# Performance work log

Hardware: AMD Instinct MI355X
Metric: run time of the kernel (lower is better)

Reference implementation:

```python
import jax, jax.numpy as jnp
import numpy as np

B, D, N = 2, 512, 2048
H, MQ, MV = 8, 64, 64
SCALE = 1.0 / np.sqrt(D).astype(np.float32)  # 1/sqrt(num_dim_q), full dim


def setup_inputs() -> dict:
    key = jax.random.key(0)
    ks = jax.random.split(key, 9)
    s = 0.02
    return {
        "Q": jax.random.normal(ks[0], (B, D, N), jnp.float32),
        "Wq": jax.random.normal(ks[1], (MQ * H, D), jnp.float32) * s,
        "bq": jnp.zeros((MQ * H,), jnp.float32),
        "Wk": jax.random.normal(ks[2], (MQ * H, D), jnp.float32) * s,
        "bk": jnp.zeros((MQ * H,), jnp.float32),
        "Wv": jax.random.normal(ks[3], (MV * H, D), jnp.float32) * s,
        "bv": jnp.zeros((MV * H,), jnp.float32),
        "Wo": jax.random.normal(ks[4], (D, MV * H), jnp.float32) * s,
        "bo": jnp.zeros((D,), jnp.float32),
    }


def _conv1x1(x, W, b):
    # Conv1d with kernel_size=1 == per-position linear: [B,Cin,N] -> [B,Cout,N]
    return jnp.einsum("bcn,oc->bon", x, W) + b[None, :, None]


def reference(Q, Wq, bq, Wk, bk, Wv, bv, Wo, bo):
    q = _conv1x1(Q, Wq, bq)  # [B, MQ*H, N]
    k = _conv1x1(Q, Wk, bk)
    v = _conv1x1(Q, Wv, bv)  # [B, MV*H, N]
    b = Q.shape[0]
    n = Q.shape[2]
    # channel index factors as (dim, head): channel = d*H + h (matches torch .view)
    q = q.reshape(b, MQ, H, n)
    k = k.reshape(b, MQ, H, n)
    v = v.reshape(b, MV, H, n)
    scores = jnp.einsum("bdhq,bdhk->bhqk", q, k) * SCALE  # [B,H,Nq,Nk]
    attn = jax.nn.softmax(scores, axis=-1)
    o = jnp.einsum("bhqk,bdhk->bdhq", attn, v)  # [B, MV, H, Nq]
    o = o.reshape(b, MV * H, n)
    return _conv1x1(o, Wo, bo)  # [B, D, N]
```

## Files before the change

### kernel.cpp

```cpp
#include <hip/hip_runtime.h>

#define DEV __device__ __forceinline__

typedef __bf16 bf16;
typedef __bf16 bf16x8 __attribute__((ext_vector_type(8)));
typedef __bf16 bf16x4 __attribute__((ext_vector_type(4)));
typedef float f32x4 __attribute__((ext_vector_type(4)));

#define B_ 2
#define D_ 512
#define N_ 2048
#define H_ 8
#define MD_ 64
#define SCALE_F (0.04419417382415922f * 1.4426950408889634f)

DEV void gload_lds16(const void* g, void* l) {
  __builtin_amdgcn_global_load_lds(
      (const __attribute__((address_space(1))) void*)g,
      (__attribute__((address_space(3))) void*)l, 16, 0, 0);
}

DEV f32x4 mfma16(bf16x8 a, bf16x8 b, f32x4 c) {
  return __builtin_amdgcn_mfma_f32_16x16x32_bf16(a, b, c, 0, 0, 0);
}

__global__ __launch_bounds__(256) void prep_w(
    const float* __restrict__ Wq, const float* __restrict__ bq,
    const float* __restrict__ Wk, const float* __restrict__ bk,
    const float* __restrict__ Wv, const float* __restrict__ bv,
    const float* __restrict__ Wo,
    bf16* __restrict__ Wf, float* __restrict__ biasf, bf16* __restrict__ Wor) {
  int row = blockIdx.x;
  int t = threadIdx.x;
  if (row < 1536) {
    const float* src;
    float scale = 1.0f;
    if (row < 512)       { src = Wq + (size_t)row * 512; scale = SCALE_F; }
    else if (row < 1024) { src = Wk + (size_t)(row - 512) * 512; }
    else                 { src = Wv + (size_t)(row - 1024) * 512; }
    for (int c = t; c < 512; c += 256)
      Wf[(size_t)row * 512 + c] = (bf16)(src[c] * scale);
    if (t == 0) {
      float bb;
      if (row < 512)       bb = bq[row] * SCALE_F;
      else if (row < 1024) bb = bk[row - 512];
      else                 bb = bv[row - 1024];
      biasf[row] = bb;
    }
  } else {
    int r = row - 1536;
    for (int c2 = t; c2 < 512; c2 += 256) {
      int hh = c2 >> 6, dd = c2 & 63;
      Wor[(size_t)r * 512 + c2] = (bf16)Wo[(size_t)r * 512 + dd * 8 + hh];
    }
  }
}

__global__ __launch_bounds__(256) void prep_qt(const float* __restrict__ Q,
                                               bf16* __restrict__ Qt) {
  __shared__ float tile[64][65];
  int b = blockIdx.z;
  int d0 = blockIdx.y * 64;
  int n0 = blockIdx.x * 64;
  int t = threadIdx.x;
  int r = t >> 2, cw = t & 3;

  const float* src = Q + ((size_t)(b * 512 + d0 + r)) * 2048 + n0 + cw * 16;
#pragma unroll
  for (int e4 = 0; e4 < 4; ++e4) {
    float4 v = *(const float4*)(src + e4 * 4);
    tile[r][cw * 16 + e4 * 4 + 0] = v.x;
    tile[r][cw * 16 + e4 * 4 + 1] = v.y;
    tile[r][cw * 16 + e4 * 4 + 2] = v.z;
    tile[r][cw * 16 + e4 * 4 + 3] = v.w;
  }
  __syncthreads();
  bf16x8 o0{}, o1{};
#pragma unroll
  for (int e = 0; e < 8; ++e) {
    o0[e] = (bf16)tile[cw * 16 + e][r];
    o1[e] = (bf16)tile[cw * 16 + 8 + e][r];
  }
  bf16* dst = Qt + ((size_t)(b * 2048 + n0 + r)) * 512 + d0 + cw * 16;
  *(bf16x8*)dst = o0;
  *((bf16x8*)dst + 1) = o1;
}

__global__ __launch_bounds__(256) void qkv_gemm(
    const bf16* __restrict__ Wf, const bf16* __restrict__ Qt,
    const float* __restrict__ biasf,
    bf16* __restrict__ qp, bf16* __restrict__ kp, bf16* __restrict__ vn) {
  __shared__ bf16 Al[128 * 32];
  __shared__ bf16 Bl[64 * 32];
  int b = blockIdx.z;
  int c0 = blockIdx.x * 128;
  int p0 = blockIdx.y * 64;
  int tid = threadIdx.x, w = tid >> 6, lane = tid & 63;
  int wm = w >> 1, wn = w & 1;
  int g = lane >> 4, l15 = lane & 15;

  const bf16* Abase = Wf + (size_t)c0 * 512;
  const bf16* Bbase = Qt + ((size_t)b * 2048 + p0) * 512;

  f32x4 acc[4][2] = {};

  for (int ks = 0; ks < 16; ++ks) {
    int k0 = ks * 32;
    __syncthreads();
#pragma unroll
    for (int i = 0; i < 2; ++i) {
      int rowl = w * 32 + i * 16 + (lane >> 2);
      gload_lds16(Abase + (size_t)rowl * 512 + k0 + (lane & 3) * 8,
                  Al + (w * 32 + i * 16) * 32);
    }
    {
      int browl = w * 16 + (lane >> 2);
      gload_lds16(Bbase + (size_t)browl * 512 + k0 + (lane & 3) * 8,
                  Bl + w * 16 * 32);
    }
    __syncthreads();
    bf16x8 a[4], bb[2];
#pragma unroll
    for (int mi = 0; mi < 4; ++mi)
      a[mi] = *(const bf16x8*)(Al + (wm * 64 + mi * 16 + l15) * 32 + g * 8);
#pragma unroll
    for (int ni = 0; ni < 2; ++ni)
      bb[ni] = *(const bf16x8*)(Bl + (wn * 32 + ni * 16 + l15) * 32 + g * 8);
#pragma unroll
    for (int mi = 0; mi < 4; ++mi)
#pragma unroll
      for (int ni = 0; ni < 2; ++ni)
        acc[mi][ni] = mfma16(a[mi], bb[ni], acc[mi][ni]);
  }

#pragma unroll
  for (int mi = 0; mi < 4; ++mi) {
#pragma unroll
    for (int ni = 0; ni < 2; ++ni) {
#pragma unroll
      for (int r = 0; r < 4; ++r) {
        int row = c0 + wm * 64 + mi * 16 + g * 4 + r;
        int p = p0 + wn * 32 + ni * 16 + l15;
        float val = acc[mi][ni][r] + biasf[row];
        bf16 hv = (bf16)val;
        if (row < 512) {
          int c = row;
          qp[(((size_t)b * 8 + (c & 7)) * 2048 + p) * 64 + (c >> 3)] = hv;
        } else if (row < 1024) {
          int c = row - 512;
          kp[(((size_t)b * 8 + (c & 7)) * 2048 + p) * 64 + (c >> 3)] = hv;
        } else {
          int c = row - 1024;
          vn[((size_t)b * 512 + c) * 2048 + p] = hv;
        }
      }
    }
  }
}

__global__ __launch_bounds__(512, 4) void attn_k(
    const bf16* __restrict__ qp, const bf16* __restrict__ kp,
    const bf16* __restrict__ vn, bf16* __restrict__ Op,
    float* __restrict__ mbuf, float* __restrict__ lbuf, int TS) {
  __shared__ bf16 Ks[2][64 * 64];
  __shared__ bf16 Vs[2][64 * 64];
  __shared__ bf16 Ps[256 * 64];
  int q0 = blockIdx.x * 256;
  int bh = blockIdx.y;
  int z = blockIdx.z;
  int b = bh >> 3, h = bh & 7;
  int tid = threadIdx.x, w = tid >> 6, lane = tid & 63;
  int g = lane >> 4, l15 = lane & 15;

  bf16x8 qreg[2][2];
#pragma unroll
  for (int rg = 0; rg < 2; ++rg)
#pragma unroll
    for (int ks2 = 0; ks2 < 2; ++ks2)
      qreg[rg][ks2] = *(const bf16x8*)(
          qp + ((size_t)bh * 2048 + q0 + w * 32 + rg * 16 + l15) * 64 +
          ks2 * 32 + g * 8);

  int krow = tid >> 3;
  int kch = (tid & 7) ^ (krow & 7);

  const bf16* Kall = kp + (size_t)bh * 2048 * 64 + (size_t)z * TS * 4096;
  const bf16* Vall = vn + ((size_t)(b * 512 + h)) * 2048 + (size_t)z * TS * 64;

  gload_lds16(Kall + (size_t)krow * 64 + kch * 8, Ks[0] + w * 512);
  gload_lds16(Vall + (size_t)krow * 16384 + kch * 8, Vs[0] + w * 512);

  f32x4 oacc[2][4] = {};
  float mrow[2] = {-1e30f, -1e30f}, rs[2] = {0.0f, 0.0f};

  __syncthreads();

  for (int t = 0; t < TS; ++t) {
    int cur = t & 1, nxt = cur ^ 1;
    int tn = (t < TS - 1) ? t + 1 : t;

    gload_lds16(Kall + (size_t)tn * 4096 + (size_t)krow * 64 + kch * 8,
                Ks[nxt] + w * 512);
    gload_lds16(Vall + (size_t)tn * 64 + (size_t)krow * 16384 + kch * 8,
                Vs[nxt] + w * 512);

    f32x4 st[2][4] = {};
    __builtin_amdgcn_s_setprio(1);
#pragma unroll
    for (int ks2 = 0; ks2 < 2; ++ks2) {
#pragma unroll
      for (int jt = 0; jt < 4; ++jt) {
        int jrow = jt * 16 + l15;
        bf16x8 kb = *(const bf16x8*)(Ks[cur] + jrow * 64 +
                                     (((ks2 * 4 + g) ^ (jrow & 7)) << 3));
        st[0][jt] = mfma16(kb, qreg[0][ks2], st[0][jt]);
        st[1][jt] = mfma16(kb, qreg[1][ks2], st[1][jt]);
      }
    }
    __builtin_amdgcn_s_setprio(0);

    float rm[2];
#pragma unroll
    for (int rg = 0; rg < 2; ++rg) {
      float m0 = st[rg][0][0];
#pragma unroll
      for (int jt = 0; jt < 4; ++jt)
#pragma unroll
        for (int i = 0; i < 4; ++i) m0 = fmaxf(m0, st[rg][jt][i]);
      m0 = fmaxf(m0, __shfl_xor(m0, 16));
      m0 = fmaxf(m0, __shfl_xor(m0, 32));
      rm[rg] = m0;
    }

    if (__any(fmaxf(rm[0] - mrow[0], rm[1] - mrow[1]) > 8.0f)) {
#pragma unroll
      for (int rg = 0; rg < 2; ++rg) {
        float nm = fmaxf(mrow[rg], rm[rg]);
        float esc = __builtin_amdgcn_exp2f(mrow[rg] - nm);
        mrow[rg] = nm;
        rs[rg] *= esc;
#pragma unroll
        for (int r = 0; r < 4; ++r) {
          float er = __shfl(esc, g * 4 + r, 64);
#pragma unroll
          for (int dt = 0; dt < 4; ++dt) oacc[rg][dt][r] *= er;
        }
      }
    }

#pragma unroll
    for (int rg = 0; rg < 2; ++rg) {
      int prow = w * 32 + rg * 16 + l15;
#pragma unroll
      for (int jt = 0; jt < 4; ++jt) {
        bf16x4 pk;
#pragma unroll
        for (int i = 0; i < 4; ++i) {
          float pv = __builtin_amdgcn_exp2f(st[rg][jt][i] - mrow[rg]);
          rs[rg] += pv;
          pk[i] = (bf16)pv;
        }
        *(bf16x4*)(Ps + prow * 64 + ((jt * 16 + g * 4) ^ ((prow & 7) << 3))) = pk;
      }
    }

    __builtin_amdgcn_s_setprio(1);
#pragma unroll
    for (int ks2 = 0; ks2 < 2; ++ks2) {
      int r0w = w * 32 + l15;
      int r1w = w * 32 + 16 + l15;
      bf16x8 pa0 = *(const bf16x8*)(Ps + r0w * 64 +
                                    (((ks2 * 4 + g) ^ (r0w & 7)) << 3));
      bf16x8 pa1 = *(const bf16x8*)(Ps + r1w * 64 +
                                    (((ks2 * 4 + g) ^ (r1w & 7)) << 3));
#pragma unroll
      for (int dt = 0; dt < 4; ++dt) {
        int drow = dt * 16 + l15;
        bf16x8 vb = *(const bf16x8*)(Vs[cur] + drow * 64 +
                                     (((ks2 * 4 + g) ^ (drow & 7)) << 3));
        oacc[0][dt] = mfma16(pa0, vb, oacc[0][dt]);
        oacc[1][dt] = mfma16(pa1, vb, oacc[1][dt]);
      }
    }
    __builtin_amdgcn_s_setprio(0);

    __syncthreads();
  }

#pragma unroll
  for (int rg = 0; rg < 2; ++rg) {
    rs[rg] += __shfl_xor(rs[rg], 16);
    rs[rg] += __shfl_xor(rs[rg], 32);
  }

  size_t zb = (size_t)(z * 16 + bh) * 2048 + q0;
#pragma unroll
  for (int rg = 0; rg < 2; ++rg) {
#pragma unroll
    for (int dt = 0; dt < 4; ++dt) {
#pragma unroll
      for (int r = 0; r < 4; ++r) {
        int i = w * 32 + rg * 16 + g * 4 + r;
        Op[(zb + i) * 64 + dt * 16 + l15] = (bf16)oacc[rg][dt][r];
      }
    }
  }
  if (lane < 16) {
#pragma unroll
    for (int rg = 0; rg < 2; ++rg) {
      int i = w * 32 + rg * 16 + l15;
      mbuf[zb + i] = mrow[rg];
      lbuf[zb + i] = rs[rg];
    }
  }
}

__global__ __launch_bounds__(256) void combine(
    const bf16* __restrict__ Op, const float* __restrict__ mbuf,
    const float* __restrict__ lbuf, bf16* __restrict__ oh, int NS) {
  int idx = blockIdx.x * 256 + threadIdx.x;
  int row = idx >> 2;
  int dc = (idx & 3) * 16;

  float M = -1e30f;
  for (int z = 0; z < NS; ++z) M = fmaxf(M, mbuf[(size_t)z * 32768 + row]);

  float L = 0.0f;
  float acc[16];
#pragma unroll
  for (int e = 0; e < 16; ++e) acc[e] = 0.0f;

  for (int z = 0; z < NS; ++z) {
    float wz = __builtin_amdgcn_exp2f(mbuf[(size_t)z * 32768 + row] - M);
    L += wz * lbuf[(size_t)z * 32768 + row];
    const bf16x8* p = (const bf16x8*)(Op + ((size_t)z * 32768 + row) * 64 + dc);
#pragma unroll
    for (int v = 0; v < 2; ++v) {
      bf16x8 x = p[v];
#pragma unroll
      for (int e = 0; e < 8; ++e) acc[v * 8 + e] += wz * (float)x[e];
    }
  }
  float invL = 1.0f / L;
  bf16x8* po = (bf16x8*)(oh + (size_t)row * 64 + dc);
#pragma unroll
  for (int v = 0; v < 2; ++v) {
    bf16x8 o;
#pragma unroll
    for (int e = 0; e < 8; ++e) o[e] = (bf16)(acc[v * 8 + e] * invL);
    po[v] = o;
  }
}

__global__ __launch_bounds__(256) void out_gemm(
    const bf16* __restrict__ Wor, const bf16* __restrict__ oh,
    const float* __restrict__ bo, float* __restrict__ out) {
  __shared__ bf16 Al[128 * 32];
  __shared__ bf16 Bl[64 * 32];
  int b = blockIdx.z;
  int r0 = blockIdx.x * 128;
  int p0 = blockIdx.y * 64;
  int tid = threadIdx.x, w = tid >> 6, lane = tid & 63;
  int wm = w >> 1, wn = w & 1;
  int g = lane >> 4, l15 = lane & 15;

  const bf16* Abase = Wor + (size_t)r0 * 512;

  f32x4 acc[4][2] = {};

  for (int ks = 0; ks < 16; ++ks) {
    int k0 = ks * 32;
    int hh = k0 >> 6, d0 = k0 & 63;
    const bf16* Bbase = oh + (((size_t)b * 8 + hh) * 2048 + p0) * 64 + d0;
    __syncthreads();
#pragma unroll
    for (int i = 0; i < 2; ++i) {
      int rowl = w * 32 + i * 16 + (lane >> 2);
      gload_lds16(Abase + (size_t)rowl * 512 + k0 + (lane & 3) * 8,
                  Al + (w * 32 + i * 16) * 32);
    }
    {
      int browl = w * 16 + (lane >> 2);
      gload_lds16(Bbase + (size_t)browl * 64 + (lane & 3) * 8,
                  Bl + w * 16 * 32);
    }
    __syncthreads();
    bf16x8 a[4], bb[2];
#pragma unroll
    for (int mi = 0; mi < 4; ++mi)
      a[mi] = *(const bf16x8*)(Al + (wm * 64 + mi * 16 + l15) * 32 + g * 8);
#pragma unroll
    for (int ni = 0; ni < 2; ++ni)
      bb[ni] = *(const bf16x8*)(Bl + (wn * 32 + ni * 16 + l15) * 32 + g * 8);
#pragma unroll
    for (int mi = 0; mi < 4; ++mi)
#pragma unroll
      for (int ni = 0; ni < 2; ++ni)
        acc[mi][ni] = mfma16(a[mi], bb[ni], acc[mi][ni]);
  }

#pragma unroll
  for (int mi = 0; mi < 4; ++mi) {
#pragma unroll
    for (int ni = 0; ni < 2; ++ni) {
#pragma unroll
      for (int r = 0; r < 4; ++r) {
        int row = r0 + wm * 64 + mi * 16 + g * 4 + r;
        int p = p0 + wn * 32 + ni * 16 + l15;
        out[((size_t)b * 512 + row) * 2048 + p] = acc[mi][ni][r] + bo[row];
      }
    }
  }
}

extern "C" void kernel_launch(void* const* d_in, const int* in_sizes, int n_in,
                              void* d_out, int out_size, void* d_ws, size_t ws_size,
                              hipStream_t stream) {
  (void)in_sizes; (void)n_in; (void)out_size;
  const float* Q  = (const float*)d_in[0];
  const float* Wq = (const float*)d_in[1];
  const float* bq = (const float*)d_in[2];
  const float* Wk = (const float*)d_in[3];
  const float* bk = (const float*)d_in[4];
  const float* Wv = (const float*)d_in[5];
  const float* bv = (const float*)d_in[6];
  const float* Wo = (const float*)d_in[7];
  const float* bo = (const float*)d_in[8];
  float* out = (float*)d_out;

  char* ws = (char*)d_ws;
  bf16*  Wf    = (bf16*)(ws + 0);
  bf16*  Wor   = (bf16*)(ws + 1572864);
  float* biasf = (float*)(ws + 2097152);
  bf16*  Qt    = (bf16*)(ws + 2103296);
  bf16*  qp    = (bf16*)(ws + 6297600);
  bf16*  kp    = (bf16*)(ws + 10491904);
  bf16*  vn    = (bf16*)(ws + 14686208);

  size_t need4 = 18880512ull + 4ull * 4194304 + 2ull * 4ull * 131072;
  int NS = (ws_size >= need4) ? 4 : 2;
  int TS = 32 / NS;

  bf16*  Opart = (bf16*)(ws + 18880512);
  float* mbuf  = (float*)(ws + 18880512 + (size_t)NS * 4194304);
  float* lbuf  = (float*)(ws + 18880512 + (size_t)NS * 4194304 +
                          (size_t)NS * 131072);
  bf16*  oh    = Opart;

  prep_w<<<dim3(2048), dim3(256), 0, stream>>>(Wq, bq, Wk, bk, Wv, bv, Wo,
                                               Wf, biasf, Wor);
  prep_qt<<<dim3(32, 8, 2), dim3(256), 0, stream>>>(Q, Qt);
  qkv_gemm<<<dim3(12, 32, 2), dim3(256), 0, stream>>>(Wf, Qt, biasf, qp, kp, vn);
  attn_k<<<dim3(8, 16, NS), dim3(512), 0, stream>>>(qp, kp, vn, Opart, mbuf,
                                                    lbuf, TS);
  combine<<<dim3(512), dim3(256), 0, stream>>>(Opart, mbuf, lbuf, oh, NS);
  out_gemm<<<dim3(4, 32, 2), dim3(256), 0, stream>>>(Wor, oh, bo, out);
}
```

Before: 83.35 us.

## Use 32x32 MFMA in attention with register-resident P via permlane swaps

The attention kernel switches from 16x16x32 to 32x32x16 bf16 MFMA tiles, so each wave holds one 32-row query block. The softmax probabilities are packed to bf16 and rearranged in registers with v_permlane32_swap, which removes the shared-memory P buffer and its write/read round trip. This also cuts LDS use and gives a single row max and sum per lane. Separately, the weight-prep and Q-transpose kernels are merged into one launch to save launch overhead. The cost is heavier accumulator register use and reliance on inline asm for the lane shuffles.

```diff
diff --git a/kernel.cpp b/kernel.cpp
--- a/kernel.cpp
+++ b/kernel.cpp
@@ -6,12 +6,9 @@
 typedef __bf16 bf16x8 __attribute__((ext_vector_type(8)));
 typedef __bf16 bf16x4 __attribute__((ext_vector_type(4)));
 typedef float f32x4 __attribute__((ext_vector_type(4)));
-
-#define B_ 2
-#define D_ 512
-#define N_ 2048
-#define H_ 8
-#define MD_ 64
+typedef float f32x16 __attribute__((ext_vector_type(16)));
+typedef unsigned int u32x4 __attribute__((ext_vector_type(4)));
+
 #define SCALE_F (0.04419417382415922f * 1.4426950408889634f)
 
 DEV void gload_lds16(const void* g, void* l) {
@@ -23,67 +20,77 @@
 DEV f32x4 mfma16(bf16x8 a, bf16x8 b, f32x4 c) {
   return __builtin_amdgcn_mfma_f32_16x16x32_bf16(a, b, c, 0, 0, 0);
 }
-
-__global__ __launch_bounds__(256) void prep_w(
+DEV f32x16 mfma32(bf16x8 a, bf16x8 b, f32x16 c) {
+  return __builtin_amdgcn_mfma_f32_32x32x16_bf16(a, b, c, 0, 0, 0);
+}
+
+DEV unsigned int pkbf(float a, float b) {
+  unsigned short ua = __builtin_bit_cast(unsigned short, (bf16)a);
+  unsigned short ub = __builtin_bit_cast(unsigned short, (bf16)b);
+  return (unsigned int)ua | ((unsigned int)ub << 16);
+}
+
+__global__ __launch_bounds__(256) void prep(
+    const float* __restrict__ Q,
     const float* __restrict__ Wq, const float* __restrict__ bq,
     const float* __restrict__ Wk, const float* __restrict__ bk,
     const float* __restrict__ Wv, const float* __restrict__ bv,
     const float* __restrict__ Wo,
-    bf16* __restrict__ Wf, float* __restrict__ biasf, bf16* __restrict__ Wor) {
-  int row = blockIdx.x;
+    bf16* __restrict__ Wf, float* __restrict__ biasf, bf16* __restrict__ Wor,
+    bf16* __restrict__ Qt) {
+  __shared__ float tile[64][65];
+  int bid = blockIdx.x;
   int t = threadIdx.x;
-  if (row < 1536) {
-    const float* src;
-    float scale = 1.0f;
-    if (row < 512)       { src = Wq + (size_t)row * 512; scale = SCALE_F; }
-    else if (row < 1024) { src = Wk + (size_t)(row - 512) * 512; }
-    else                 { src = Wv + (size_t)(row - 1024) * 512; }
-    for (int c = t; c < 512; c += 256)
-      Wf[(size_t)row * 512 + c] = (bf16)(src[c] * scale);
-    if (t == 0) {
-      float bb;
-      if (row < 512)       bb = bq[row] * SCALE_F;
-      else if (row < 1024) bb = bk[row - 512];
-      else                 bb = bv[row - 1024];
-      biasf[row] = bb;
+  if (bid < 2048) {
+    int row = bid;
+    if (row < 1536) {
+      const float* src;
+      float scale = 1.0f;
+      if (row < 512)       { src = Wq + (size_t)row * 512; scale = SCALE_F; }
+      else if (row < 1024) { src = Wk + (size_t)(row - 512) * 512; }
+      else                 { src = Wv + (size_t)(row - 1024) * 512; }
+      for (int c = t; c < 512; c += 256)
+        Wf[(size_t)row * 512 + c] = (bf16)(src[c] * scale);
+      if (t == 0) {
+        float bb;
+        if (row < 512)       bb = bq[row] * SCALE_F;
+        else if (row < 1024) bb = bk[row - 512];
+        else                 bb = bv[row - 1024];
+        biasf[row] = bb;
+      }
+    } else {
+      int r = row - 1536;
+      for (int c2 = t; c2 < 512; c2 += 256) {
+        int hh = c2 >> 6, dd = c2 & 63;
+        Wor[(size_t)r * 512 + c2] = (bf16)Wo[(size_t)r * 512 + dd * 8 + hh];
+      }
     }
   } else {
-    int r = row - 1536;
-    for (int c2 = t; c2 < 512; c2 += 256) {
-      int hh = c2 >> 6, dd = c2 & 63;
-      Wor[(size_t)r * 512 + c2] = (bf16)Wo[(size_t)r * 512 + dd * 8 + hh];
-    }
-  }
-}
-
-__global__ __launch_bounds__(256) void prep_qt(const float* __restrict__ Q,
-                                               bf16* __restrict__ Qt) {
-  __shared__ float tile[64][65];
-  int b = blockIdx.z;
-  int d0 = blockIdx.y * 64;
-  int n0 = blockIdx.x * 64;
-  int t = threadIdx.x;
-  int r = t >> 2, cw = t & 3;
-
-  const float* src = Q + ((size_t)(b * 512 + d0 + r)) * 2048 + n0 + cw * 16;
-#pragma unroll
-  for (int e4 = 0; e4 < 4; ++e4) {
-    float4 v = *(const float4*)(src + e4 * 4);
-    tile[r][cw * 16 + e4 * 4 + 0] = v.x;
-    tile[r][cw * 16 + e4 * 4 + 1] = v.y;
-    tile[r][cw * 16 + e4 * 4 + 2] = v.z;
-    tile[r][cw * 16 + e4 * 4 + 3] = v.w;
-  }
-  __syncthreads();
-  bf16x8 o0{}, o1{};
-#pragma unroll
-  for (int e = 0; e < 8; ++e) {
-    o0[e] = (bf16)tile[cw * 16 + e][r];
-    o1[e] = (bf16)tile[cw * 16 + 8 + e][r];
-  }
-  bf16* dst = Qt + ((size_t)(b * 2048 + n0 + r)) * 512 + d0 + cw * 16;
-  *(bf16x8*)dst = o0;
-  *((bf16x8*)dst + 1) = o1;
+    int id2 = bid - 2048;
+    int n0 = (id2 & 31) * 64;
+    int d0 = ((id2 >> 5) & 7) * 64;
+    int b = id2 >> 8;
+    int r = t >> 2, cw = t & 3;
+    const float* src = Q + ((size_t)(b * 512 + d0 + r)) * 2048 + n0 + cw * 16;
+#pragma unroll
+    for (int e4 = 0; e4 < 4; ++e4) {
+      float4 v = *(const float4*)(src + e4 * 4);
+      tile[r][cw * 16 + e4 * 4 + 0] = v.x;
+      tile[r][cw * 16 + e4 * 4 + 1] = v.y;
+      tile[r][cw * 16 + e4 * 4 + 2] = v.z;
+      tile[r][cw * 16 + e4 * 4 + 3] = v.w;
+    }
+    __syncthreads();
+    bf16x8 o0{}, o1{};
+#pragma unroll
+    for (int e = 0; e < 8; ++e) {
+      o0[e] = (bf16)tile[cw * 16 + e][r];
+      o1[e] = (bf16)tile[cw * 16 + 8 + e][r];
+    }
+    bf16* dst = Qt + ((size_t)(b * 2048 + n0 + r)) * 512 + d0 + cw * 16;
+    *(bf16x8*)dst = o0;
+    *((bf16x8*)dst + 1) = o1;
+  }
 }
 
 __global__ __launch_bounds__(256) void qkv_gemm(
@@ -164,22 +171,18 @@
     float* __restrict__ mbuf, float* __restrict__ lbuf, int TS) {
   __shared__ bf16 Ks[2][64 * 64];
   __shared__ bf16 Vs[2][64 * 64];
-  __shared__ bf16 Ps[256 * 64];
   int q0 = blockIdx.x * 256;
   int bh = blockIdx.y;
   int z = blockIdx.z;
   int b = bh >> 3, h = bh & 7;
   int tid = threadIdx.x, w = tid >> 6, lane = tid & 63;
-  int g = lane >> 4, l15 = lane & 15;
-
-  bf16x8 qreg[2][2];
-#pragma unroll
-  for (int rg = 0; rg < 2; ++rg)
-#pragma unroll
-    for (int ks2 = 0; ks2 < 2; ++ks2)
-      qreg[rg][ks2] = *(const bf16x8*)(
-          qp + ((size_t)bh * 2048 + q0 + w * 32 + rg * 16 + l15) * 64 +
-          ks2 * 32 + g * 8);
+  int l31 = lane & 31, hi = lane >> 5;
+
+  bf16x8 qreg[4];
+#pragma unroll
+  for (int kd = 0; kd < 4; ++kd)
+    qreg[kd] = *(const bf16x8*)(
+        qp + ((size_t)bh * 2048 + q0 + w * 32 + l31) * 64 + kd * 16 + hi * 8);
 
   int krow = tid >> 3;
   int kch = (tid & 7) ^ (krow & 7);
@@ -190,8 +193,8 @@
   gload_lds16(Kall + (size_t)krow * 64 + kch * 8, Ks[0] + w * 512);
   gload_lds16(Vall + (size_t)krow * 16384 + kch * 8, Vs[0] + w * 512);
 
-  f32x4 oacc[2][4] = {};
-  float mrow[2] = {-1e30f, -1e30f}, rs[2] = {0.0f, 0.0f};
+  f32x16 oacc0 = {}, oacc1 = {};
+  float mrow = -1e30f, rs = 0.0f;
 
   __syncthreads();
 
@@ -204,114 +207,88 @@
     gload_lds16(Vall + (size_t)tn * 64 + (size_t)krow * 16384 + kch * 8,
                 Vs[nxt] + w * 512);
 
-    f32x4 st[2][4] = {};
+    f32x16 st0 = {}, st1 = {};
     __builtin_amdgcn_s_setprio(1);
 #pragma unroll
-    for (int ks2 = 0; ks2 < 2; ++ks2) {
-#pragma unroll
-      for (int jt = 0; jt < 4; ++jt) {
-        int jrow = jt * 16 + l15;
-        bf16x8 kb = *(const bf16x8*)(Ks[cur] + jrow * 64 +
-                                     (((ks2 * 4 + g) ^ (jrow & 7)) << 3));
-        st[0][jt] = mfma16(kb, qreg[0][ks2], st[0][jt]);
-        st[1][jt] = mfma16(kb, qreg[1][ks2], st[1][jt]);
-      }
+    for (int kd = 0; kd < 4; ++kd) {
+      int sw = ((kd * 2 + hi) ^ (l31 & 7)) << 3;
+      bf16x8 kb0 = *(const bf16x8*)(Ks[cur] + l31 * 64 + sw);
+      bf16x8 kb1 = *(const bf16x8*)(Ks[cur] + (32 + l31) * 64 + sw);
+      st0 = mfma32(kb0, qreg[kd], st0);
+      st1 = mfma32(kb1, qreg[kd], st1);
     }
     __builtin_amdgcn_s_setprio(0);
 
-    float rm[2];
-#pragma unroll
-    for (int rg = 0; rg < 2; ++rg) {
-      float m0 = st[rg][0][0];
-#pragma unroll
-      for (int jt = 0; jt < 4; ++jt)
-#pragma unroll
-        for (int i = 0; i < 4; ++i) m0 = fmaxf(m0, st[rg][jt][i]);
-      m0 = fmaxf(m0, __shfl_xor(m0, 16));
-      m0 = fmaxf(m0, __shfl_xor(m0, 32));
-      rm[rg] = m0;
-    }
-
-    if (__any(fmaxf(rm[0] - mrow[0], rm[1] - mrow[1]) > 8.0f)) {
-#pragma unroll
-      for (int rg = 0; rg < 2; ++rg) {
-        float nm = fmaxf(mrow[rg], rm[rg]);
-        float esc = __builtin_amdgcn_exp2f(mrow[rg] - nm);
-        mrow[rg] = nm;
-        rs[rg] *= esc;
-#pragma unroll
-        for (int r = 0; r < 4; ++r) {
-          float er = __shfl(esc, g * 4 + r, 64);
-#pragma unroll
-          for (int dt = 0; dt < 4; ++dt) oacc[rg][dt][r] *= er;
-        }
-      }
-    }
-
-#pragma unroll
-    for (int rg = 0; rg < 2; ++rg) {
-      int prow = w * 32 + rg * 16 + l15;
-#pragma unroll
-      for (int jt = 0; jt < 4; ++jt) {
-        bf16x4 pk;
-#pragma unroll
-        for (int i = 0; i < 4; ++i) {
-          float pv = __builtin_amdgcn_exp2f(st[rg][jt][i] - mrow[rg]);
-          rs[rg] += pv;
-          pk[i] = (bf16)pv;
-        }
-        *(bf16x4*)(Ps + prow * 64 + ((jt * 16 + g * 4) ^ ((prow & 7) << 3))) = pk;
-      }
+    float rm = st0[0];
+#pragma unroll
+    for (int r = 1; r < 16; ++r) rm = fmaxf(rm, st0[r]);
+#pragma unroll
+    for (int r = 0; r < 16; ++r) rm = fmaxf(rm, st1[r]);
+    rm = fmaxf(rm, __shfl_xor(rm, 32));
+
+    if (__any(rm > mrow + 8.0f)) {
+      float nm = fmaxf(mrow, rm);
+      float esc = __builtin_amdgcn_exp2f(mrow - nm);
+      mrow = nm;
+      rs *= esc;
+#pragma unroll
+      for (int r = 0; r < 16; ++r) {
+        int ql = (r & 3) + 8 * (r >> 2) + 4 * hi;
+        float er = __shfl(esc, ql, 64);
+        oacc0[r] *= er;
+        oacc1[r] *= er;
+      }
+    }
+
+    bf16x8 pa[4];
+#pragma unroll
+    for (int tile = 0; tile < 2; ++tile) {
+      float pv[16];
+#pragma unroll
+      for (int r = 0; r < 16; ++r) {
+        float v = __builtin_amdgcn_exp2f((tile ? st1[r] : st0[r]) - mrow);
+        pv[r] = v;
+        rs += v;
+      }
+      unsigned int r0d0 = pkbf(pv[0], pv[1]),   r0d1 = pkbf(pv[2], pv[3]);
+      unsigned int r1d0 = pkbf(pv[4], pv[5]),   r1d1 = pkbf(pv[6], pv[7]);
+      unsigned int r2d0 = pkbf(pv[8], pv[9]),   r2d1 = pkbf(pv[10], pv[11]);
+      unsigned int r3d0 = pkbf(pv[12], pv[13]), r3d1 = pkbf(pv[14], pv[15]);
+      asm volatile("v_permlane32_swap_b32 %0, %1" : "+v"(r0d0), "+v"(r1d0));
+      asm volatile("v_permlane32_swap_b32 %0, %1" : "+v"(r0d1), "+v"(r1d1));
+      pa[tile * 2] = __builtin_bit_cast(bf16x8, (u32x4){r0d0, r0d1, r1d0, r1d1});
+      asm volatile("v_permlane32_swap_b32 %0, %1" : "+v"(r2d0), "+v"(r3d0));
+      asm volatile("v_permlane32_swap_b32 %0, %1" : "+v"(r2d1), "+v"(r3d1));
+      pa[tile * 2 + 1] =
+          __builtin_bit_cast(bf16x8, (u32x4){r2d0, r2d1, r3d0, r3d1});
     }
 
     __builtin_amdgcn_s_setprio(1);
 #pragma unroll
-    for (int ks2 = 0; ks2 < 2; ++ks2) {
-      int r0w = w * 32 + l15;
-      int r1w = w * 32 + 16 + l15;
-      bf16x8 pa0 = *(const bf16x8*)(Ps + r0w * 64 +
-                                    (((ks2 * 4 + g) ^ (r0w & 7)) << 3));
-      bf16x8 pa1 = *(const bf16x8*)(Ps + r1w * 64 +
-                                    (((ks2 * 4 + g) ^ (r1w & 7)) << 3));
-#pragma unroll
-      for (int dt = 0; dt < 4; ++dt) {
-        int drow = dt * 16 + l15;
-        bf16x8 vb = *(const bf16x8*)(Vs[cur] + drow * 64 +
-                                     (((ks2 * 4 + g) ^ (drow & 7)) << 3));
-        oacc[0][dt] = mfma16(pa0, vb, oacc[0][dt]);
-        oacc[1][dt] = mfma16(pa1, vb, oacc[1][dt]);
-      }
+    for (int kt = 0; kt < 4; ++kt) {
+      int sw0 = ((kt * 2 + hi) ^ (l31 & 7)) << 3;
+      bf16x8 vb0 = *(const bf16x8*)(Vs[cur] + l31 * 64 + sw0);
+      bf16x8 vb1 = *(const bf16x8*)(Vs[cur] + (32 + l31) * 64 + sw0);
+      oacc0 = mfma32(pa[kt], vb0, oacc0);
+      oacc1 = mfma32(pa[kt], vb1, oacc1);
     }
     __builtin_amdgcn_s_setprio(0);
 
     __syncthreads();
   }
 
-#pragma unroll
-  for (int rg = 0; rg < 2; ++rg) {
-    rs[rg] += __shfl_xor(rs[rg], 16);
-    rs[rg] += __shfl_xor(rs[rg], 32);
-  }
-
-  size_t zb = (size_t)(z * 16 + bh) * 2048 + q0;
-#pragma unroll
-  for (int rg = 0; rg < 2; ++rg) {
-#pragma unroll
-    for (int dt = 0; dt < 4; ++dt) {
-#pragma unroll
-      for (int r = 0; r < 4; ++r) {
-        int i = w * 32 + rg * 16 + g * 4 + r;
-        Op[(zb + i) * 64 + dt * 16 + l15] = (bf16)oacc[rg][dt][r];
-      }
-    }
-  }
-  if (lane < 16) {
-#pragma unroll
-    for (int rg = 0; rg < 2; ++rg) {
-      int i = w * 32 + rg * 16 + l15;
-      mbuf[zb + i] = mrow[rg];
-      lbuf[zb + i] = rs[rg];
-    }
+  rs += __shfl_xor(rs, 32);
+
+  size_t zb = (size_t)(z * 16 + bh) * 2048 + q0 + w * 32;
+#pragma unroll
+  for (int r = 0; r < 16; ++r) {
+    int ql = (r & 3) + 8 * (r >> 2) + 4 * hi;
+    Op[(zb + ql) * 64 + l31] = (bf16)oacc0[r];
+    Op[(zb + ql) * 64 + 32 + l31] = (bf16)oacc1[r];
+  }
+  if (hi == 0) {
+    mbuf[zb + l31] = mrow;
+    lbuf[zb + l31] = rs;
   }
 }
 
@@ -447,9 +424,8 @@
                           (size_t)NS * 131072);
   bf16*  oh    = Opart;
 
-  prep_w<<<dim3(2048), dim3(256), 0, stream>>>(Wq, bq, Wk, bk, Wv, bv, Wo,
-                                               Wf, biasf, Wor);
-  prep_qt<<<dim3(32, 8, 2), dim3(256), 0, stream>>>(Q, Qt);
+  prep<<<dim3(2560), dim3(256), 0, stream>>>(Q, Wq, bq, Wk, bk, Wv, bv, Wo,
+                                             Wf, biasf, Wor, Qt);
   qkv_gemm<<<dim3(12, 32, 2), dim3(256), 0, stream>>>(Wf, Qt, biasf, qp, kp, vn);
   attn_k<<<dim3(8, 16, NS), dim3(512), 0, stream>>>(qp, kp, vn, Opart, mbuf,
                                                     lbuf, TS);
```

Measured after the change: 80.43 us. -3.5%, faster.
